# Performance work log

Hardware: AMD Instinct MI355X
Metric: run time of the kernel (lower is better)

The kernel has to match this reference:

```python
import jax, jax.numpy as jnp
import numpy as np

B, S, D, H = 2, 2048, 1024, 16
DK = D // H


def setup_inputs() -> dict:
    key = jax.random.key(0)
    ks = jax.random.split(key, 9)
    sc = 0.02
    return {
        "x": jax.random.normal(ks[0], (B, S, D), dtype=jnp.float32),
        "attention_mask": jnp.ones((B, S), dtype=jnp.int32),
        "Wq": jax.random.normal(ks[1], (D, D), dtype=jnp.float32) * sc,
        "bq": jax.random.normal(ks[2], (D,), dtype=jnp.float32) * sc,
        "Wk": jax.random.normal(ks[3], (D, D), dtype=jnp.float32) * sc,
        "bk": jax.random.normal(ks[4], (D,), dtype=jnp.float32) * sc,
        "Wv": jax.random.normal(ks[5], (D, D), dtype=jnp.float32) * sc,
        "bv": jax.random.normal(ks[6], (D,), dtype=jnp.float32) * sc,
        "Wo": jax.random.normal(ks[7], (D, D), dtype=jnp.float32) * sc,
        "bo": jax.random.normal(ks[8], (D,), dtype=jnp.float32) * sc,
    }


def reference(x, attention_mask, Wq, bq, Wk, bk, Wv, bv, Wo, bo):
    b, s, d = x.shape
    # projections (Linear: x @ W + b) then split heads -> [b, h, s, dk]
    def heads(t):
        return t.reshape(b, s, H, DK).transpose(0, 2, 1, 3)
    Q = heads(x @ Wq + bq)
    K = heads(x @ Wk + bk)
    V = heads(x @ Wv + bv)
    # NOTE: original computes K @ Q^T (not Q @ K^T) and applies NO 1/sqrt(dk) scale
    scores = jnp.einsum("bhid,bhjd->bhij", K, Q)  # [b, h, s, s]
    causal = jnp.tril(jnp.ones((s, s), dtype=bool))  # [s, s]
    final_mask = attention_mask[:, None, None, :].astype(bool) & causal[None, None]
    scores = jnp.where(final_mask, scores, -jnp.inf)
    attn = jax.nn.softmax(scores, axis=-1)
    out = jnp.einsum("bhij,bhjd->bhid", attn, V)  # [b, h, s, dk]
    out = out.transpose(0, 2, 1, 3).reshape(b, s, d)
    return out @ Wo + bo
```

## Files before the change

kernel.cpp:

```cpp
#include <hip/hip_runtime.h>
#include <stdint.h>
#include <stddef.h>


typedef short bf16x8 __attribute__((ext_vector_type(8)));
typedef float f32x4  __attribute__((ext_vector_type(4)));

__device__ __forceinline__ short f2bf(float f) {
  union { float f; uint32_t u; } a; a.f = f;
  uint32_t r = a.u + 0x7fffu + ((a.u >> 16) & 1u);
  return (short)(r >> 16);
}
__device__ __forceinline__ float bf2f(short s) {
  union { uint32_t u; float f; } a; a.u = ((uint32_t)(uint16_t)s) << 16;
  return a.f;
}
__device__ __forceinline__ uint32_t pack2bf(float a, float b) {
  union { float f; uint32_t u; } x, y; x.f = a; y.f = b;
  return (x.u >> 16) | (y.u & 0xffff0000u);
}
__device__ __forceinline__ float fast_exp2(float x) {
#if __has_builtin(__builtin_amdgcn_exp2f)
  return __builtin_amdgcn_exp2f(x);
#else
  return exp2f(x);
#endif
}
__device__ __forceinline__ void async16(const void* g, void* l) {
  __builtin_amdgcn_global_load_lds(
      (const __attribute__((address_space(1))) uint32_t*)g,
      (__attribute__((address_space(3))) uint32_t*)l, 16, 0, 0);
}
#define MFMA(a, b, c) __builtin_amdgcn_mfma_f32_16x16x32_bf16((a), (b), (c), 0, 0, 0)

__global__ void k_split_x(const float* __restrict__ x, short* __restrict__ xhi) {
  int i = blockIdx.x * 256 + threadIdx.x;
  float4 v = ((const float4*)x)[i];
  short4 h;
  h.x = f2bf(v.x);
  h.y = f2bf(v.y);
  h.z = f2bf(v.z);
  h.w = f2bf(v.w);
  ((short4*)xhi)[i] = h;
}

__global__ void k_prep_w(const float* __restrict__ Wq, const float* __restrict__ Wk,
                         const float* __restrict__ Wv, const float* __restrict__ Wo,
                         short* __restrict__ whi, short* __restrict__ wo) {
  __shared__ float T[64][65];
  int z = blockIdx.z;
  const float* W = (z == 0) ? Wq : (z == 1) ? Wk : (z == 2) ? Wv : Wo;
  int n0 = blockIdx.x * 64, k0 = blockIdx.y * 64;
  int t = threadIdx.x;
  int rr = t >> 4, cc = (t & 15) * 4;
#pragma unroll
  for (int it = 0; it < 4; ++it) {
    int row = rr + it * 16;
    float4 v = *(const float4*)&W[(size_t)(k0 + row) * 1024 + n0 + cc];
    T[row][cc] = v.x; T[row][cc + 1] = v.y; T[row][cc + 2] = v.z; T[row][cc + 3] = v.w;
  }
  __syncthreads();
  short* oh = (z < 3) ? (whi + (size_t)z * 1048576) : wo;
#pragma unroll
  for (int it = 0; it < 4; ++it) {
    int nrow = rr + it * 16;
    short4 h4;
    h4.x = f2bf(T[cc + 0][nrow]);
    h4.y = f2bf(T[cc + 1][nrow]);
    h4.z = f2bf(T[cc + 2][nrow]);
    h4.w = f2bf(T[cc + 3][nrow]);
    *(short4*)&oh[(size_t)(n0 + nrow) * 1024 + k0 + cc] = h4;
  }
}

__global__ __launch_bounds__(256, 3) void k_gemm_qkv(
    const short* __restrict__ xhi, const short* __restrict__ whi,
    const float* __restrict__ bq, const float* __restrict__ bk,
    const float* __restrict__ bv,
    short* __restrict__ Qhi, short* __restrict__ Qlo,
    short* __restrict__ Khi, short* __restrict__ Klo,
    short* __restrict__ Vt) {
  __shared__ short AH[2][4096];
  __shared__ short BH[2][4096];
  int tid = threadIdx.x;
  int bx = blockIdx.x;
  int m0 = blockIdx.y * 128;
  int n0g = bx * 128;
  int w = tid >> 6, lane = tid & 63, lr = lane & 15, lq = lane >> 4;
  int wm = w >> 1, wn = w & 1;
  int z = bx >> 3;
  f32x4 acc[4][4] = {};

  auto stage = [&](int ks, int pb) {
#pragma unroll
    for (int it = 0; it < 2; ++it) {
      int idx = it * 256 + tid;
      int row = idx >> 2, c = idx & 3;
      int cs = c ^ (row & 3);
      async16(xhi + (size_t)(m0 + row) * 1024 + ks * 32 + cs * 8, &AH[pb][idx * 8]);
      async16(whi + (size_t)(n0g + row) * 1024 + ks * 32 + cs * 8, &BH[pb][idx * 8]);
    }
  };

  stage(0, 0);
  int p = 0;
  int g = lq ^ (lr & 3);
  if (z == 2) {
    for (int ks = 0; ks < 32; ++ks) {
      __syncthreads();
      if (ks < 31) stage(ks + 1, p ^ 1);
      const bf16x8* A8 = (const bf16x8*)AH[p];
      const bf16x8* B8 = (const bf16x8*)BH[p];
      bf16x8 af[4], bfr[4];
#pragma unroll
      for (int mt = 0; mt < 4; ++mt) af[mt] = A8[(wm * 64 + mt * 16 + lr) * 4 + g];
#pragma unroll
      for (int nt = 0; nt < 4; ++nt) bfr[nt] = B8[(wn * 64 + nt * 16 + lr) * 4 + g];
#pragma unroll
      for (int mt = 0; mt < 4; ++mt)
#pragma unroll
        for (int nt = 0; nt < 4; ++nt)
          acc[mt][nt] = MFMA(af[mt], bfr[nt], acc[mt][nt]);
      p ^= 1;
    }
#pragma unroll
    for (int nt = 0; nt < 4; ++nt) {
      int dg = (n0g & 1023) + wn * 64 + nt * 16 + lr;
      float bvv = bv[dg];
      int hh = dg >> 6, dk = dg & 63;
#pragma unroll
      for (int mt = 0; mt < 4; ++mt) {
        int row = m0 + wm * 64 + mt * 16 + lq * 4;
        int b_ = row >> 11, s_ = row & 2047;
        short4 pk;
        pk.x = f2bf(acc[mt][nt][0] + bvv);
        pk.y = f2bf(acc[mt][nt][1] + bvv);
        pk.z = f2bf(acc[mt][nt][2] + bvv);
        pk.w = f2bf(acc[mt][nt][3] + bvv);
        *(short4*)&Vt[(size_t)((b_ * 16 + hh) * 64 + dk) * 2048 + s_] = pk;
      }
    }
  } else {
    for (int ks = 0; ks < 32; ++ks) {
      __syncthreads();
      if (ks < 31) stage(ks + 1, p ^ 1);
      const bf16x8* A8 = (const bf16x8*)AH[p];
      const bf16x8* B8 = (const bf16x8*)BH[p];
      bf16x8 af[4], bfr[4];
#pragma unroll
      for (int mt = 0; mt < 4; ++mt) af[mt] = A8[(wm * 64 + mt * 16 + lr) * 4 + g];
#pragma unroll
      for (int nt = 0; nt < 4; ++nt) bfr[nt] = B8[(wn * 64 + nt * 16 + lr) * 4 + g];
#pragma unroll
      for (int mt = 0; mt < 4; ++mt)
#pragma unroll
        for (int nt = 0; nt < 4; ++nt)
          acc[mt][nt] = MFMA(bfr[nt], af[mt], acc[mt][nt]);
      p ^= 1;
    }
    const float LOG2E = 1.44269504f;
    const float* bias = (z == 0) ? bq : bk;
    short* Ch = (z == 0) ? Qhi : Khi;
    short* Cl = (z == 0) ? Qlo : Klo;
#pragma unroll
    for (int mt = 0; mt < 4; ++mt) {
      int row = m0 + wm * 64 + mt * 16 + lr;
#pragma unroll
      for (int nt = 0; nt < 4; ++nt) {
        int colg = (n0g & 1023) + wn * 64 + nt * 16 + lq * 4;
        float4 b4 = *(const float4*)&bias[colg];
        float v0 = acc[mt][nt][0] + b4.x;
        float v1 = acc[mt][nt][1] + b4.y;
        float v2 = acc[mt][nt][2] + b4.z;
        float v3 = acc[mt][nt][3] + b4.w;
        if (z == 0) { v0 *= LOG2E; v1 *= LOG2E; v2 *= LOG2E; v3 *= LOG2E; }
        short4 hi4, lo4;
        hi4.x = f2bf(v0); lo4.x = f2bf(v0 - bf2f(hi4.x));
        hi4.y = f2bf(v1); lo4.y = f2bf(v1 - bf2f(hi4.y));
        hi4.z = f2bf(v2); lo4.z = f2bf(v2 - bf2f(hi4.z));
        hi4.w = f2bf(v3); lo4.w = f2bf(v3 - bf2f(hi4.w));
        size_t o = (size_t)row * 1024 + colg;
        *(short4*)&Ch[o] = hi4;
        if (z == 1) *(short4*)&Cl[o] = lo4;
      }
    }
  }
}

__global__ __launch_bounds__(256, 3) void k_gemm_o(
    const short* __restrict__ Ab, const short* __restrict__ Bb,
    const float* __restrict__ bias, float* __restrict__ Cf) {
  __shared__ short AH[2][4096];
  __shared__ short BH[2][4096];
  int tid = threadIdx.x;
  int m0 = blockIdx.y * 128, n0 = blockIdx.x * 128;
  int w = tid >> 6, lane = tid & 63, lr = lane & 15, lq = lane >> 4;
  int wm = w >> 1, wn = w & 1;
  f32x4 acc[4][4] = {};

  auto stage = [&](int ks, int pb) {
#pragma unroll
    for (int it = 0; it < 2; ++it) {
      int idx = it * 256 + tid;
      int row = idx >> 2, c = idx & 3;
      int cs = c ^ (row & 3);
      async16(Ab + (size_t)(m0 + row) * 1024 + ks * 32 + cs * 8, &AH[pb][idx * 8]);
      async16(Bb + (size_t)(n0 + row) * 1024 + ks * 32 + cs * 8, &BH[pb][idx * 8]);
    }
  };

  stage(0, 0);
  int p = 0;
  int g = lq ^ (lr & 3);
  for (int ks = 0; ks < 32; ++ks) {
    __syncthreads();
    if (ks < 31) stage(ks + 1, p ^ 1);
    const bf16x8* A8 = (const bf16x8*)AH[p];
    const bf16x8* B8 = (const bf16x8*)BH[p];
    bf16x8 af[4], bfr[4];
#pragma unroll
    for (int mt = 0; mt < 4; ++mt) af[mt] = A8[(wm * 64 + mt * 16 + lr) * 4 + g];
#pragma unroll
    for (int nt = 0; nt < 4; ++nt) bfr[nt] = B8[(wn * 64 + nt * 16 + lr) * 4 + g];
#pragma unroll
    for (int mt = 0; mt < 4; ++mt)
#pragma unroll
      for (int nt = 0; nt < 4; ++nt)
        acc[mt][nt] = MFMA(bfr[nt], af[mt], acc[mt][nt]);
    p ^= 1;
  }

#pragma unroll
  for (int mt = 0; mt < 4; ++mt) {
    int row = m0 + wm * 64 + mt * 16 + lr;
#pragma unroll
    for (int nt = 0; nt < 4; ++nt) {
      int colg = n0 + wn * 64 + nt * 16 + lq * 4;
      float4 b4 = *(const float4*)&bias[colg];
      float4 o4;
      o4.x = acc[mt][nt][0] + b4.x;
      o4.y = acc[mt][nt][1] + b4.y;
      o4.z = acc[mt][nt][2] + b4.z;
      o4.w = acc[mt][nt][3] + b4.w;
      *(float4*)&Cf[(size_t)row * 1024 + colg] = o4;
    }
  }
}

__global__ __launch_bounds__(256, 4) void k_attn(
    const short* __restrict__ Khi, const short* __restrict__ Klo,
    const short* __restrict__ Qhi, const short* __restrict__ Vt,
    const int* __restrict__ amask, short* __restrict__ Obuf,
    float* __restrict__ PA, float* __restrict__ PB,
    float* __restrict__ LA, float* __restrict__ LB) {
  __shared__ short QH[2][4096];
  __shared__ short VS[2][4096];
  int tid = threadIdx.x;
  int bid = blockIdx.x;
  int xcd = bid & 7, i2 = bid >> 3;
  int bh = xcd * 4 + (i2 & 3);
  int o  = i2 >> 2;
  int P, t0, t1;
  bool partial, slotB = false;
  if (o < 16) {
    P = 16 + o; t0 = 0; t1 = 16; partial = true;
  } else {
    int q = o - 16, lvl = q >> 1;
    if (q & 1) {
      P = 15 - lvl; t0 = 0; t1 = P + 1; partial = false;
    } else {
      P = 31 - lvl; t0 = 16; t1 = P + 1; partial = true; slotB = true;
    }
  }
  int b = bh >> 4, h = bh & 15;
  int w = tid >> 6, lane = tid & 63, lr = lane & 15, lq = lane >> 4;
  int band = 2 * P + (w >> 1);
  int rb0 = band * 32 + (w & 1) * 16;

  bf16x8 kh[2], kl[2];
  {
    size_t ra = ((size_t)(b * 2048 + rb0 + lr)) * 1024 + h * 64;
#pragma unroll
    for (int ks = 0; ks < 2; ++ks) {
      kh[ks] = *(const bf16x8*)(Khi + ra + ks * 32 + lq * 8);
      kl[ks] = *(const bf16x8*)(Klo + ra + ks * 32 + lq * 8);
    }
  }

  f32x4 O[4] = {};
  float ls = 0.f;
  int iq = rb0 + lr;
  int baddr0 = (((lq & 1) * 2) * 16 + lr) * 4;
  int baddr1 = baddr0 + 64;

  auto stage = [&](int jt, int pb) {
    int j0 = jt * 64;
#pragma unroll
    for (int it = 0; it < 2; ++it) {
      int idx2 = it * 256 + tid;
      int rr = idx2 >> 3, c = idx2 & 7;
      int cs = c ^ (rr & 7);
      size_t gq = ((size_t)(b * 2048 + j0 + rr)) * 1024 + h * 64 + cs * 8;
      async16(Qhi + gq, &QH[pb][idx2 * 8]);
      size_t gv = ((size_t)(bh * 64 + rr)) * 2048 + j0 + cs * 8;
      async16(Vt + gv, &VS[pb][idx2 * 8]);
    }
  };

  stage(t0, 0);
  int p = 0;
  for (int t = t0; t < t1; ++t) {
    __syncthreads();
    if (t + 1 < t1) stage(t + 1, p ^ 1);
    int j0 = t * 64;
    const bf16x8* Q8 = (const bf16x8*)QH[p];
    const bf16x8* V8 = (const bf16x8*)VS[p];

    int av = amask[b * 2048 + j0 + lane];
    unsigned long long bal = __ballot(av != 0);
    bool allv = (bal == ~0ull);

    f32x4 s[4] = {};
#pragma unroll
    for (int mt = 0; mt < 4; ++mt) {
      int row = mt * 16 + lr;
#pragma unroll
      for (int ks = 0; ks < 2; ++ks) {
        int gi = row * 8 + ((ks * 4 + lq) ^ (row & 7));
        bf16x8 qa = Q8[gi];
        s[mt] = MFMA(qa, kh[ks], s[mt]);
        s[mt] = MFMA(qa, kl[ks], s[mt]);
      }
    }

    bool diag = (t == P);
    float pv[4][4];
#pragma unroll
    for (int mt = 0; mt < 4; ++mt)
#pragma unroll
      for (int r = 0; r < 4; ++r)
        pv[mt][r] = fast_exp2(s[mt][r]);
    if (diag) {
#pragma unroll
      for (int mt = 0; mt < 4; ++mt)
#pragma unroll
        for (int r = 0; r < 4; ++r)
          if (j0 + mt * 16 + lq * 4 + r > iq) pv[mt][r] = 0.f;
    }
    if (!allv) {
#pragma unroll
      for (int mt = 0; mt < 4; ++mt)
#pragma unroll
        for (int r = 0; r < 4; ++r)
          if (!((bal >> (mt * 16 + lq * 4 + r)) & 1)) pv[mt][r] = 0.f;
    }
    uint32_t pd[4][2];
#pragma unroll
    for (int mt = 0; mt < 4; ++mt) {
      ls += (pv[mt][0] + pv[mt][1]) + (pv[mt][2] + pv[mt][3]);
      pd[mt][0] = pack2bf(pv[mt][0], pv[mt][1]);
      pd[mt][1] = pack2bf(pv[mt][2], pv[mt][3]);
    }

#pragma unroll
    for (int k2 = 0; k2 < 2; ++k2) {
      union { int i[4]; bf16x8 v; } pa;
#pragma unroll
      for (int dd = 0; dd < 4; ++dd) {
        int addr = (dd >> 1) ? baddr1 : baddr0;
        int v0 = __builtin_amdgcn_ds_bpermute(addr, (int)pd[k2 * 2 + 0][dd & 1]);
        int v1 = __builtin_amdgcn_ds_bpermute(addr, (int)pd[k2 * 2 + 1][dd & 1]);
        pa.i[dd] = (lq >> 1) ? v1 : v0;
      }
#pragma unroll
      for (int nt = 0; nt < 4; ++nt) {
        int row = nt * 16 + lr;
        bf16x8 vb = V8[row * 8 + ((k2 * 4 + lq) ^ (row & 7))];
        O[nt] = MFMA(pa.v, vb, O[nt]);
      }
    }
    p ^= 1;
  }

  float tsum = ls;
  tsum += __shfl_xor(tsum, 16);
  tsum += __shfl_xor(tsum, 32);

  if (!partial) {
    float inv[4];
#pragma unroll
    for (int r = 0; r < 4; ++r) inv[r] = 1.0f / __shfl(tsum, lq * 4 + r, 64);
#pragma unroll
    for (int nt = 0; nt < 4; ++nt)
#pragma unroll
      for (int r = 0; r < 4; ++r) {
        int row = b * 2048 + rb0 + lq * 4 + r;
        int col = h * 64 + nt * 16 + lr;
        Obuf[(size_t)row * 1024 + col] = f2bf(O[nt][r] * inv[r]);
      }
  } else {
    float* PO = slotB ? PB : PA;
    float* PL = slotB ? LB : LA;
    int prb = bh * 1024 + (P - 16) * 64 + w * 16;
#pragma unroll
    for (int nt = 0; nt < 4; ++nt)
#pragma unroll
      for (int r = 0; r < 4; ++r)
        PO[(size_t)(prb + lq * 4 + r) * 64 + nt * 16 + lr] = O[nt][r];
    if (lq == 0) PL[prb + lr] = tsum;
  }
}

__global__ void k_merge(const float* __restrict__ PA, const float* __restrict__ PB,
                        const float* __restrict__ LA, const float* __restrict__ LB,
                        short* __restrict__ Obuf) {
  int t = blockIdx.x * 256 + threadIdx.x;
  int pr = t >> 4, cg = t & 15;
  float4 a = ((const float4*)PA)[pr * 16 + cg];
  float4 bb4 = ((const float4*)PB)[pr * 16 + cg];
  float inv = 1.0f / (LA[pr] + LB[pr]);
  int bh = pr >> 10, P = 16 + ((pr >> 6) & 15), loc = pr & 63;
  int b = bh >> 4, h = bh & 15;
  size_t addr = ((size_t)(b * 2048 + P * 64 + loc)) * 1024 + h * 64 + cg * 4;
  short4 oq;
  oq.x = f2bf((a.x + bb4.x) * inv);
  oq.y = f2bf((a.y + bb4.y) * inv);
  oq.z = f2bf((a.z + bb4.z) * inv);
  oq.w = f2bf((a.w + bb4.w) * inv);
  *(short4*)&Obuf[addr] = oq;
}

extern "C" void kernel_launch(void* const* d_in, const int* in_sizes, int n_in,
                              void* d_out, int out_size, void* d_ws, size_t ws_size,
                              hipStream_t stream) {
  const float* x  = (const float*)d_in[0];
  const int* amask = (const int*)d_in[1];
  const float* Wq = (const float*)d_in[2];
  const float* bq = (const float*)d_in[3];
  const float* Wk = (const float*)d_in[4];
  const float* bk = (const float*)d_in[5];
  const float* Wv = (const float*)d_in[6];
  const float* bv = (const float*)d_in[7];
  const float* Wo = (const float*)d_in[8];
  const float* bo = (const float*)d_in[9];

  char* ws = (char*)d_ws;
  const size_t MB = 1024 * 1024;
  short* xhi = (short*)(ws);
  float* PA  = (float*)(ws + 8 * MB);
  short* whi = (short*)(ws + 16 * MB);
  float* LA  = (float*)(ws + 22 * MB);
  float* LB  = (float*)(ws + 23 * MB);
  short* wo  = (short*)(ws + 26 * MB);
  short* Qhi = (short*)(ws + 28 * MB);
  float* PB  = (float*)(ws + 36 * MB);
  short* Qlo = (short*)(ws + 36 * MB);
  short* Khi = (short*)(ws + 44 * MB);
  short* Klo = (short*)(ws + 52 * MB);
  short* Vt  = (short*)(ws + 60 * MB);
  short* Obuf = xhi;

  k_split_x<<<4096, 256, 0, stream>>>(x, xhi);
  k_prep_w<<<dim3(16, 16, 4), 256, 0, stream>>>(Wq, Wk, Wv, Wo, whi, wo);

  k_gemm_qkv<<<dim3(24, 32), 256, 0, stream>>>(xhi, whi, bq, bk, bv,
                                               Qhi, Qlo, Khi, Klo, Vt);
  k_attn<<<1536, 256, 0, stream>>>(Khi, Klo, Qhi, Vt, amask, Obuf,
                                   PA, PB, LA, LB);
  k_merge<<<2048, 256, 0, stream>>>(PA, PB, LA, LB, Obuf);
  k_gemm_o<<<dim3(8, 32), 256, 0, stream>>>(Obuf, wo, bo, (float*)d_out);
}
```

Before: 202.5 us.

## Fuse split-KV merge into attention via atomic pair counter; merge prep kernels

Removes the separate k_merge kernel. Each partial attention block now writes its partial output and sum, then bumps a per-pair atomic counter, and whichever block finishes second reads the other partial and writes the normalized bf16 output. Also fuses the x conversion and weight transpose kernels into one launch that also zeroes the flags. This saves two kernel launches and a round trip of partial data through a separate pass, at the cost of threadfence/atomic synchronisation and a serial tail in the finishing block.

```diff
diff --git a/kernel.cpp b/kernel.cpp
--- a/kernel.cpp
+++ b/kernel.cpp
@@ -33,43 +33,50 @@
 }
 #define MFMA(a, b, c) __builtin_amdgcn_mfma_f32_16x16x32_bf16((a), (b), (c), 0, 0, 0)
 
-__global__ void k_split_x(const float* __restrict__ x, short* __restrict__ xhi) {
-  int i = blockIdx.x * 256 + threadIdx.x;
-  float4 v = ((const float4*)x)[i];
-  short4 h;
-  h.x = f2bf(v.x);
-  h.y = f2bf(v.y);
-  h.z = f2bf(v.z);
-  h.w = f2bf(v.w);
-  ((short4*)xhi)[i] = h;
-}
-
-__global__ void k_prep_w(const float* __restrict__ Wq, const float* __restrict__ Wk,
-                         const float* __restrict__ Wv, const float* __restrict__ Wo,
-                         short* __restrict__ whi, short* __restrict__ wo) {
+__global__ void k_prep(const float* __restrict__ x, short* __restrict__ xhi,
+                       const float* __restrict__ Wq, const float* __restrict__ Wk,
+                       const float* __restrict__ Wv, const float* __restrict__ Wo,
+                       short* __restrict__ whi, short* __restrict__ wo,
+                       int* __restrict__ flags) {
   __shared__ float T[64][65];
-  int z = blockIdx.z;
-  const float* W = (z == 0) ? Wq : (z == 1) ? Wk : (z == 2) ? Wv : Wo;
-  int n0 = blockIdx.x * 64, k0 = blockIdx.y * 64;
+  int bid = blockIdx.x;
   int t = threadIdx.x;
-  int rr = t >> 4, cc = (t & 15) * 4;
-#pragma unroll
-  for (int it = 0; it < 4; ++it) {
-    int row = rr + it * 16;
-    float4 v = *(const float4*)&W[(size_t)(k0 + row) * 1024 + n0 + cc];
-    T[row][cc] = v.x; T[row][cc + 1] = v.y; T[row][cc + 2] = v.z; T[row][cc + 3] = v.w;
-  }
-  __syncthreads();
-  short* oh = (z < 3) ? (whi + (size_t)z * 1048576) : wo;
-#pragma unroll
-  for (int it = 0; it < 4; ++it) {
-    int nrow = rr + it * 16;
-    short4 h4;
-    h4.x = f2bf(T[cc + 0][nrow]);
-    h4.y = f2bf(T[cc + 1][nrow]);
-    h4.z = f2bf(T[cc + 2][nrow]);
-    h4.w = f2bf(T[cc + 3][nrow]);
-    *(short4*)&oh[(size_t)(n0 + nrow) * 1024 + k0 + cc] = h4;
+  if (bid < 4096) {
+    int i = bid * 256 + t;
+    float4 v = ((const float4*)x)[i];
+    short4 h;
+    h.x = f2bf(v.x);
+    h.y = f2bf(v.y);
+    h.z = f2bf(v.z);
+    h.w = f2bf(v.w);
+    ((short4*)xhi)[i] = h;
+  } else if (bid < 5120) {
+    int i = bid - 4096;
+    int bx = i & 15, by = (i >> 4) & 15, z = i >> 8;
+    const float* W = (z == 0) ? Wq : (z == 1) ? Wk : (z == 2) ? Wv : Wo;
+    int n0 = bx * 64, k0 = by * 64;
+    int rr = t >> 4, cc = (t & 15) * 4;
+#pragma unroll
+    for (int it = 0; it < 4; ++it) {
+      int row = rr + it * 16;
+      float4 v = *(const float4*)&W[(size_t)(k0 + row) * 1024 + n0 + cc];
+      T[row][cc] = v.x; T[row][cc + 1] = v.y; T[row][cc + 2] = v.z; T[row][cc + 3] = v.w;
+    }
+    __syncthreads();
+    short* oh = (z < 3) ? (whi + (size_t)z * 1048576) : wo;
+#pragma unroll
+    for (int it = 0; it < 4; ++it) {
+      int nrow = rr + it * 16;
+      short4 h4;
+      h4.x = f2bf(T[cc + 0][nrow]);
+      h4.y = f2bf(T[cc + 1][nrow]);
+      h4.z = f2bf(T[cc + 2][nrow]);
+      h4.w = f2bf(T[cc + 3][nrow]);
+      *(short4*)&oh[(size_t)(n0 + nrow) * 1024 + k0 + cc] = h4;
+    }
+  } else {
+    flags[t] = 0;
+    flags[t + 256] = 0;
   }
 }
 
@@ -252,7 +259,8 @@
     const short* __restrict__ Qhi, const short* __restrict__ Vt,
     const int* __restrict__ amask, short* __restrict__ Obuf,
     float* __restrict__ PA, float* __restrict__ PB,
-    float* __restrict__ LA, float* __restrict__ LB) {
+    float* __restrict__ LA, float* __restrict__ LB,
+    int* __restrict__ flags) {
   __shared__ short QH[2][4096];
   __shared__ short VS[2][4096];
   int tid = threadIdx.x;
@@ -401,33 +409,40 @@
   } else {
     float* PO = slotB ? PB : PA;
     float* PL = slotB ? LB : LA;
-    int prb = bh * 1024 + (P - 16) * 64 + w * 16;
+    const float* PO_o = slotB ? PA : PB;
+    const float* PL_o = slotB ? LA : LB;
+    int pairIdx = bh * 16 + (P - 16);
+    int prb = pairIdx * 64 + w * 16;
 #pragma unroll
     for (int nt = 0; nt < 4; ++nt)
 #pragma unroll
       for (int r = 0; r < 4; ++r)
         PO[(size_t)(prb + lq * 4 + r) * 64 + nt * 16 + lr] = O[nt][r];
     if (lq == 0) PL[prb + lr] = tsum;
-  }
-}
-
-__global__ void k_merge(const float* __restrict__ PA, const float* __restrict__ PB,
-                        const float* __restrict__ LA, const float* __restrict__ LB,
-                        short* __restrict__ Obuf) {
-  int t = blockIdx.x * 256 + threadIdx.x;
-  int pr = t >> 4, cg = t & 15;
-  float4 a = ((const float4*)PA)[pr * 16 + cg];
-  float4 bb4 = ((const float4*)PB)[pr * 16 + cg];
-  float inv = 1.0f / (LA[pr] + LB[pr]);
-  int bh = pr >> 10, P = 16 + ((pr >> 6) & 15), loc = pr & 63;
-  int b = bh >> 4, h = bh & 15;
-  size_t addr = ((size_t)(b * 2048 + P * 64 + loc)) * 1024 + h * 64 + cg * 4;
-  short4 oq;
-  oq.x = f2bf((a.x + bb4.x) * inv);
-  oq.y = f2bf((a.y + bb4.y) * inv);
-  oq.z = f2bf((a.z + bb4.z) * inv);
-  oq.w = f2bf((a.w + bb4.w) * inv);
-  *(short4*)&Obuf[addr] = oq;
+    __threadfence();
+    __syncthreads();
+    __shared__ int oldSh;
+    if (tid == 0) oldSh = atomicAdd(&flags[pairIdx], 1);
+    __syncthreads();
+    if (oldSh == 1) {
+      __threadfence();
+      float osum = PL_o[prb + lr];
+      float tot = tsum + osum;
+      float inv[4];
+#pragma unroll
+      for (int r = 0; r < 4; ++r) inv[r] = 1.0f / __shfl(tot, lq * 4 + r, 64);
+#pragma unroll
+      for (int nt = 0; nt < 4; ++nt)
+#pragma unroll
+        for (int r = 0; r < 4; ++r) {
+          float oo = O[nt][r] +
+                     PO_o[(size_t)(prb + lq * 4 + r) * 64 + nt * 16 + lr];
+          int row = b * 2048 + rb0 + lq * 4 + r;
+          int col = h * 64 + nt * 16 + lr;
+          Obuf[(size_t)row * 1024 + col] = f2bf(oo * inv[r]);
+        }
+    }
+  }
 }
 
 extern "C" void kernel_launch(void* const* d_in, const int* in_sizes, int n_in,
@@ -451,6 +466,7 @@
   short* whi = (short*)(ws + 16 * MB);
   float* LA  = (float*)(ws + 22 * MB);
   float* LB  = (float*)(ws + 23 * MB);
+  int*  flags = (int*)(ws + 24 * MB);
   short* wo  = (short*)(ws + 26 * MB);
   short* Qhi = (short*)(ws + 28 * MB);
   float* PB  = (float*)(ws + 36 * MB);
@@ -460,13 +476,10 @@
   short* Vt  = (short*)(ws + 60 * MB);
   short* Obuf = xhi;
 
-  k_split_x<<<4096, 256, 0, stream>>>(x, xhi);
-  k_prep_w<<<dim3(16, 16, 4), 256, 0, stream>>>(Wq, Wk, Wv, Wo, whi, wo);
-
+  k_prep<<<5121, 256, 0, stream>>>(x, xhi, Wq, Wk, Wv, Wo, whi, wo, flags);
   k_gemm_qkv<<<dim3(24, 32), 256, 0, stream>>>(xhi, whi, bq, bk, bv,
                                                Qhi, Qlo, Khi, Klo, Vt);
   k_attn<<<1536, 256, 0, stream>>>(Khi, Klo, Qhi, Vt, amask, Obuf,
-                                   PA, PB, LA, LB);
-  k_merge<<<2048, 256, 0, stream>>>(PA, PB, LA, LB, Obuf);
+                                   PA, PB, LA, LB, flags);
   k_gemm_o<<<dim3(8, 32), 256, 0, stream>>>(Obuf, wo, bo, (float*)d_out);
 }
```

Measured after the change: 379.6 us. 87.5% more time.
